# Kernel tuning notes

Hardware: AMD Instinct MI355X
Metric: run time of the kernel (lower is better)

The kernel has to match this reference:

```python
import jax, jax.numpy as jnp
import numpy as np

N = 100_000        # nodes
E = 1_600_000      # edges (avg degree 16)
NODE_DIM = 64
HIDDEN = 64
OUT = 32


def _glorot(key, fan_in, fan_out):
    lim = np.sqrt(6.0 / (fan_in + fan_out)).astype(np.float32)
    return jax.random.uniform(key, (fan_in, fan_out), jnp.float32, -lim, lim)


def setup_inputs() -> dict:
    key = jax.random.key(0)
    ks = jax.random.split(key, 5)
    x = jax.random.normal(ks[0], (N, NODE_DIM), jnp.float32)
    edge_index = jax.random.randint(ks[1], (2, E), 0, N, dtype=jnp.int64)
    return {
        "x": x,
        "edge_index": edge_index,
        "W1": _glorot(ks[2], NODE_DIM, HIDDEN),
        "b1": jnp.zeros((HIDDEN,), jnp.float32),
        "Wmu": _glorot(ks[3], HIDDEN, OUT),
        "bmu": jnp.zeros((OUT,), jnp.float32),
        "Wlv": _glorot(ks[4], HIDDEN, OUT),
        "blv": jnp.zeros((OUT,), jnp.float32),
    }


def _gcn_conv(h, W, b, src, dst, norm, n):
    """PyG GCNConv: linear (no bias) -> normalized scatter-add -> + bias.
    src/dst/norm already include self-loops and deg^{-1/2} symmetric norm."""
    h = h @ W                                   # [n, out]
    msg = h[src] * norm[:, None]                # [E+N, out] gather
    out = jax.ops.segment_sum(msg, dst, num_segments=n)  # scatter-add
    return out + b


def reference(x, edge_index, W1, b1, Wmu, bmu, Wlv, blv):
    loops = jnp.arange(N, dtype=edge_index.dtype)
    src = jnp.concatenate([edge_index[0], loops])  # add self-loops
    dst = jnp.concatenate([edge_index[1], loops])
    # symmetric normalization: deg computed on target nodes (all weights 1)
    deg = jax.ops.segment_sum(jnp.ones_like(src, dtype=x.dtype), dst, num_segments=N)
    dinv = jax.lax.rsqrt(deg)                   # deg >= 1 due to self-loops
    norm = dinv[src] * dinv[dst]

    h = jax.nn.relu(_gcn_conv(x, W1, b1, src, dst, norm, N))
    mu = _gcn_conv(h, Wmu, bmu, src, dst, norm, N)
    logvar = _gcn_conv(h, Wlv, blv, src, dst, norm, N)
    return mu, logvar
```

## Files before the change

### kernel.cpp

```cpp
#include <hip/hip_runtime.h>
#include <hip/hip_fp16.h>


#define BKT_SHIFT 9
#define BKT_NODES 512
#define CHUNK 2048

typedef __attribute__((ext_vector_type(8))) _Float16 half8;
typedef __attribute__((ext_vector_type(4))) float float4v;
typedef __attribute__((ext_vector_type(4))) unsigned uint4v;

__device__ __forceinline__ int imin(int a, int b) { return a < b ? a : b; }
__device__ __forceinline__ int imax(int a, int b) { return a > b ? a : b; }
__device__ __forceinline__ unsigned h2u(__half2 v) {
  union { __half2 h; unsigned u; } c; c.h = v; return c.u;
}
__device__ __forceinline__ __half2 u2h(unsigned x) {
  union { unsigned u; __half2 h; } c; c.u = x; return c.h;
}

__global__ __launch_bounds__(256) void bucket_count(const int* __restrict__ dst,
                                                    int* __restrict__ cnt,
                                                    int E, int nbk, int nblk) {
  __shared__ int hist[2][256];
  const int t = threadIdx.x;
  const int h = (t >> 7) & 1;
  hist[0][t] = 0;
  hist[1][t] = 0;
  __syncthreads();
  const int base = blockIdx.x * CHUNK;
  const int end = imin(base + CHUNK, E);
  for (int e = base + t * 4; e < end; e += 1024) {
    if (e + 3 < end) {
      const int4 d4 = *(const int4*)(dst + e);
      atomicAdd(&hist[h][d4.x >> BKT_SHIFT], 1);
      atomicAdd(&hist[h][d4.y >> BKT_SHIFT], 1);
      atomicAdd(&hist[h][d4.z >> BKT_SHIFT], 1);
      atomicAdd(&hist[h][d4.w >> BKT_SHIFT], 1);
    } else {
      for (int k = e; k < end; ++k) atomicAdd(&hist[h][dst[k] >> BKT_SHIFT], 1);
    }
  }
  __syncthreads();
  if (t < nbk) cnt[t * nblk + blockIdx.x] = hist[0][t] + hist[1][t];
}

__global__ __launch_bounds__(256) void scan_rows(int* __restrict__ cnt,
                                                 int* __restrict__ rowsum,
                                                 int nbk, int nblk) {
  __shared__ int red[256];
  const int b = blockIdx.x;
  const int t = threadIdx.x;
  const int rbase = b * nblk;
  int vals[4];
  int run = 0;
#pragma unroll
  for (int k = 0; k < 4; ++k) {
    const int idx = t * 4 + k;
    const int v = (idx < nblk) ? cnt[rbase + idx] : 0;
    vals[k] = v;
    run += v;
  }
  red[t] = run;
  __syncthreads();
  for (int off = 1; off < 256; off <<= 1) {
    const int u = (t >= off) ? red[t - off] : 0;
    __syncthreads();
    red[t] += u;
    __syncthreads();
  }
  int acc = red[t] - run;
  if (t == 255) rowsum[b] = red[255];
#pragma unroll
  for (int k = 0; k < 4; ++k) {
    const int idx = t * 4 + k;
    if (idx < nblk) {
      cnt[rbase + idx] = acc;
      acc += vals[k];
    }
  }
}

__global__ __launch_bounds__(256) void bucket_scatter(const int* __restrict__ src,
                                                      const int* __restrict__ dst,
                                                      const int* __restrict__ cnt,
                                                      const int* __restrict__ rowsum,
                                                      int* __restrict__ tmp,
                                                      int E, int nbk, int nblk) {
  __shared__ int cur[256];
  __shared__ int red[256];
  const int t = threadIdx.x;
  const int c = blockIdx.x;
  const int v = (t < nbk) ? rowsum[t] : 0;
  red[t] = v;
  __syncthreads();
  for (int off = 1; off < 256; off <<= 1) {
    const int u = (t >= off) ? red[t - off] : 0;
    __syncthreads();
    red[t] += u;
    __syncthreads();
  }
  if (t < nbk) cur[t] = (red[t] - v) + cnt[t * nblk + c];
  __syncthreads();
  const int base = c * CHUNK;
  const int end = imin(base + CHUNK, E);
  for (int e = base + t * 4; e < end; e += 1024) {
    if (e + 3 < end) {
      const int4 s4 = *(const int4*)(src + e);
      const int4 d4 = *(const int4*)(dst + e);
      int p0 = atomicAdd(&cur[d4.x >> BKT_SHIFT], 1);
      tmp[p0] = (s4.x << 9) | (d4.x & 511);
      int p1 = atomicAdd(&cur[d4.y >> BKT_SHIFT], 1);
      tmp[p1] = (s4.y << 9) | (d4.y & 511);
      int p2 = atomicAdd(&cur[d4.z >> BKT_SHIFT], 1);
      tmp[p2] = (s4.z << 9) | (d4.z & 511);
      int p3 = atomicAdd(&cur[d4.w >> BKT_SHIFT], 1);
      tmp[p3] = (s4.w << 9) | (d4.w & 511);
    } else {
      for (int k = e; k < end; ++k) {
        const int d = dst[k];
        const int pos = atomicAdd(&cur[d >> BKT_SHIFT], 1);
        tmp[pos] = (src[k] << 9) | (d & 511);
      }
    }
  }
}

__global__ __launch_bounds__(1024) void bucket_build(const int* __restrict__ tmp,
                                                     const int* __restrict__ rowsum,
                                                     int* __restrict__ row_ptr,
                                                     int* __restrict__ pairs,
                                                     const float* __restrict__ x,
                                                     __half* __restrict__ xs,
                                                     __half* __restrict__ hs,
                                                     int n, int nbk, int E) {
  __shared__ int hist[BKT_NODES];
  __shared__ int scn[BKT_NODES];
  __shared__ int red[256];
  __shared__ int s_sh, e_sh;
  const int b = blockIdx.x;
  const int t = threadIdx.x;
  const int node0 = b << BKT_SHIFT;
  int v0 = 0;
  if (t < 256) {
    v0 = (t < nbk) ? rowsum[t] : 0;
    red[t] = v0;
  }
  if (t < BKT_NODES) hist[t] = 0;
  __syncthreads();
  for (int off = 1; off < 256; off <<= 1) {
    int u = 0;
    if (t < 256 && t >= off) u = red[t - off];
    __syncthreads();
    if (t < 256) red[t] += u;
    __syncthreads();
  }
  if (t == 0) {
    const int incl = red[b];
    e_sh = incl;
    s_sh = incl - rowsum[b];
  }
  __syncthreads();
  const int s = s_sh;
  const int e = e_sh;
  for (int k = s + t; k < e; k += 1024) atomicAdd(&hist[tmp[k] & 511], 1);
  __syncthreads();
  int v = 0;
  if (t < BKT_NODES) {
    v = hist[t];
    scn[t] = v;
  }
  __syncthreads();
  for (int off = 1; off < BKT_NODES; off <<= 1) {
    int u = 0;
    if (t < BKT_NODES && t >= off) u = scn[t - off];
    __syncthreads();
    if (t < BKT_NODES) scn[t] += u;
    __syncthreads();
  }
  if (t < BKT_NODES) {
    const int excl = s + scn[t] - v;
    const int node = node0 + t;
    if (node < n) row_ptr[node] = excl;
    if (b == nbk - 1 && t == 0) row_ptr[n] = E;
    hist[t] = excl;
    scn[t] = __float_as_int(rsqrtf(1.0f + (float)v));
  }
  __syncthreads();
  for (int k = s + t; k < e; k += 1024) {
    const int w = tmp[k];
    const int pos = atomicAdd(&hist[w & 511], 1);
    pairs[pos] = w >> 9;
  }
  const int nloc = imin(BKT_NODES, n - node0);
  for (int idx = t; idx < nloc * 16; idx += 1024) {
    const int nl = idx >> 4, f4 = idx & 15;
    const float4 v4 = ((const float4*)x)[(size_t)(node0 + nl) * 16 + f4];
    const float d = __int_as_float(scn[nl]);
    __half2* o = (__half2*)(xs + (size_t)(node0 + nl) * 64 + f4 * 4);
    o[0] = __floats2half2_rn(d * v4.x, d * v4.y);
    o[1] = __floats2half2_rn(d * v4.z, d * v4.w);
  }
  if (b == 0 && t < 32) {
    if (t < 16)
      ((float2*)(xs + (size_t)n * 64))[t] = make_float2(0.f, 0.f);
    else
      ((float2*)(hs + (size_t)n * 64))[t - 16] = make_float2(0.f, 0.f);
  }
}


#define YSTRIDE 264

__global__ __launch_bounds__(256, 4) void agg_layer1(const __half* __restrict__ xs,
                                                     const int* __restrict__ pairs,
                                                     const int* __restrict__ row_ptr,
                                                     const float* __restrict__ W1,
                                                     const float* __restrict__ b1,
                                                     __half* __restrict__ hs, int n) {
  __shared__ _Float16 ylds_all[4][16 * YSTRIDE];
  __shared__ float dilds_all[4][16];
  const int wv = threadIdx.x >> 6;
  _Float16* ylds = ylds_all[wv];
  float* dilds = dilds_all[wv];
  const int lane = threadIdx.x & 63;
  const int g = lane >> 3, q = lane & 7;
  const int quad = lane >> 4, col = lane & 15;

  half8 bfrag[2][4];
#pragma unroll
  for (int s = 0; s < 2; ++s)
#pragma unroll
    for (int t = 0; t < 4; ++t)
#pragma unroll
      for (int jj = 0; jj < 8; ++jj)
        bfrag[s][t][jj] = (_Float16)W1[(s * 32 + quad * 8 + jj) * 64 + t * 16 + col];
  float bias[4];
#pragma unroll
  for (int t = 0; t < 4; ++t) bias[t] = b1[t * 16 + col];

  const int ntiles = (n + 15) >> 4;
  for (int tile = blockIdx.x * 4 + wv; tile < ntiles; tile += gridDim.x * 4) {
    const int row0 = tile << 4;
#pragma unroll 1
    for (int rg = 0; rg < 4; ++rg) {
      int start[4], end[4], idx[4];
      __half2 acc[4][4];
      int maxdeg = 0;
#pragma unroll
      for (int j = 0; j < 4; ++j) {
        const int i = row0 + rg * 4 + j;
        start[j] = 0; end[j] = 0;
        if (i < n) { start[j] = row_ptr[i]; end[j] = row_ptr[i + 1]; }
        maxdeg = imax(maxdeg, end[j] - start[j]);
#pragma unroll
        for (int k = 0; k < 4; ++k) acc[j][k] = u2h(0u);
        idx[j] = (start[j] + g < end[j]) ? pairs[start[j] + g] : n;
      }
      const int iters = (maxdeg + 7) >> 3;
#pragma unroll 1
      for (int it = 0; it < iters; ++it) {
        int nidx[4];
#pragma unroll
        for (int j = 0; j < 4; ++j) {
          const int ofs2 = start[j] + (it + 1) * 8 + g;
          nidx[j] = (ofs2 < end[j]) ? pairs[ofs2] : n;
        }
#pragma unroll
        for (int j = 0; j < 4; ++j) {
          const float4 rr = *(const float4*)(xs + (size_t)idx[j] * 64 + q * 8);
          const __half2* hp = (const __half2*)&rr;
#pragma unroll
          for (int k = 0; k < 4; ++k) acc[j][k] = __hadd2(acc[j][k], hp[k]);
        }
#pragma unroll
        for (int j = 0; j < 4; ++j) idx[j] = nidx[j];
      }
#pragma unroll
      for (int j = 0; j < 4; ++j) {
        const int i = row0 + rg * 4 + j;
        if (g == 0 && i < n) {
          const float4 sr = *(const float4*)(xs + (size_t)i * 64 + q * 8);
          const __half2* hp = (const __half2*)&sr;
#pragma unroll
          for (int k = 0; k < 4; ++k) acc[j][k] = __hadd2(acc[j][k], hp[k]);
        }
#pragma unroll
        for (int k = 0; k < 4; ++k) {
          unsigned u = __shfl_xor(h2u(acc[j][k]), 32);
          acc[j][k] = __hadd2(acc[j][k], u2h(u));
        }
        const float di = rsqrtf((float)(1 + end[j] - start[j]));
        const __half hdi = __float2half(di);
        const __half2 di2 = __halves2half2(hdi, hdi);
        uint4v st;
        st.x = h2u(__hmul2(di2, acc[j][0]));
        st.y = h2u(__hmul2(di2, acc[j][1]));
        st.z = h2u(__hmul2(di2, acc[j][2]));
        st.w = h2u(__hmul2(di2, acc[j][3]));
        *(uint4v*)(ylds + (rg * 4 + j) * YSTRIDE + (g & 3) * 64 + q * 8) = st;
        if (lane == 0) dilds[rg * 4 + j] = di;
      }
    }
    float4v acc[4];
#pragma unroll
    for (int t = 0; t < 4; ++t) acc[t] = (float4v){bias[t], bias[t], bias[t], bias[t]};
#pragma unroll
    for (int s2 = 0; s2 < 8; ++s2) {
      half8 af = *(half8*)(ylds + col * YSTRIDE + s2 * 32 + quad * 8);
      const int sW = s2 & 1;
#pragma unroll
      for (int t = 0; t < 4; ++t)
        acc[t] = __builtin_amdgcn_mfma_f32_16x16x32_f16(af, bfrag[sW][t], acc[t], 0, 0, 0);
    }
    const float4 dis = *(const float4*)(dilds + quad * 4);
    const float dd[4] = {dis.x, dis.y, dis.z, dis.w};
#pragma unroll
    for (int t = 0; t < 4; ++t)
#pragma unroll
      for (int reg = 0; reg < 4; ++reg) {
        const int row = row0 + quad * 4 + reg;
        if (row < n)
          hs[(size_t)row * 64 + t * 16 + col] =
              __float2half(dd[reg] * fmaxf(acc[t][reg], 0.f));
      }
  }
}

__global__ __launch_bounds__(256, 4) void agg_layer2(const __half* __restrict__ hsin,
                                                     const int* __restrict__ pairs,
                                                     const int* __restrict__ row_ptr,
                                                     const float* __restrict__ Wmu,
                                                     const float* __restrict__ bmu,
                                                     const float* __restrict__ Wlv,
                                                     const float* __restrict__ blv,
                                                     float* __restrict__ out_mu,
                                                     float* __restrict__ out_lv, int n) {
  __shared__ _Float16 ylds_all[4][16 * YSTRIDE];
  const int wv = threadIdx.x >> 6;
  _Float16* ylds = ylds_all[wv];
  const int lane = threadIdx.x & 63;
  const int g = lane >> 3, q = lane & 7;
  const int quad = lane >> 4, col = lane & 15;

  half8 bfrag[2][4];
#pragma unroll
  for (int s = 0; s < 2; ++s)
#pragma unroll
    for (int t = 0; t < 4; ++t) {
      const int j = t * 16 + col;
      const float* W = (j < 32) ? Wmu : Wlv;
      const int jc = j & 31;
#pragma unroll
      for (int jj = 0; jj < 8; ++jj)
        bfrag[s][t][jj] = (_Float16)W[(s * 32 + quad * 8 + jj) * 32 + jc];
    }
  float bias[4];
#pragma unroll
  for (int t = 0; t < 4; ++t) {
    const int j = t * 16 + col;
    bias[t] = (j < 32) ? bmu[j] : blv[j - 32];
  }

  const int ntiles = (n + 15) >> 4;
  for (int tile = blockIdx.x * 4 + wv; tile < ntiles; tile += gridDim.x * 4) {
    const int row0 = tile << 4;
#pragma unroll 1
    for (int rg = 0; rg < 4; ++rg) {
      int start[4], end[4], idx[4];
      __half2 acc[4][4];
      int maxdeg = 0;
#pragma unroll
      for (int j = 0; j < 4; ++j) {
        const int i = row0 + rg * 4 + j;
        start[j] = 0; end[j] = 0;
        if (i < n) { start[j] = row_ptr[i]; end[j] = row_ptr[i + 1]; }
        maxdeg = imax(maxdeg, end[j] - start[j]);
#pragma unroll
        for (int k = 0; k < 4; ++k) acc[j][k] = u2h(0u);
        idx[j] = (start[j] + g < end[j]) ? pairs[start[j] + g] : n;
      }
      const int iters = (maxdeg + 7) >> 3;
#pragma unroll 1
      for (int it = 0; it < iters; ++it) {
        int nidx[4];
#pragma unroll
        for (int j = 0; j < 4; ++j) {
          const int ofs2 = start[j] + (it + 1) * 8 + g;
          nidx[j] = (ofs2 < end[j]) ? pairs[ofs2] : n;
        }
#pragma unroll
        for (int j = 0; j < 4; ++j) {
          const float4 rr = *(const float4*)(hsin + (size_t)idx[j] * 64 + q * 8);
          const __half2* hp = (const __half2*)&rr;
#pragma unroll
          for (int k = 0; k < 4; ++k) acc[j][k] = __hadd2(acc[j][k], hp[k]);
        }
#pragma unroll
        for (int j = 0; j < 4; ++j) idx[j] = nidx[j];
      }
#pragma unroll
      for (int j = 0; j < 4; ++j) {
        const int i = row0 + rg * 4 + j;
        if (g == 0 && i < n) {
          const float4 sr = *(const float4*)(hsin + (size_t)i * 64 + q * 8);
          const __half2* hp = (const __half2*)&sr;
#pragma unroll
          for (int k = 0; k < 4; ++k) acc[j][k] = __hadd2(acc[j][k], hp[k]);
        }
#pragma unroll
        for (int k = 0; k < 4; ++k) {
          unsigned u = __shfl_xor(h2u(acc[j][k]), 32);
          acc[j][k] = __hadd2(acc[j][k], u2h(u));
        }
        const float di = rsqrtf((float)(1 + end[j] - start[j]));
        const __half hdi = __float2half(di);
        const __half2 di2 = __halves2half2(hdi, hdi);
        uint4v st;
        st.x = h2u(__hmul2(di2, acc[j][0]));
        st.y = h2u(__hmul2(di2, acc[j][1]));
        st.z = h2u(__hmul2(di2, acc[j][2]));
        st.w = h2u(__hmul2(di2, acc[j][3]));
        *(uint4v*)(ylds + (rg * 4 + j) * YSTRIDE + (g & 3) * 64 + q * 8) = st;
      }
    }
    float4v acc[4];
#pragma unroll
    for (int t = 0; t < 4; ++t) acc[t] = (float4v){bias[t], bias[t], bias[t], bias[t]};
#pragma unroll
    for (int s2 = 0; s2 < 8; ++s2) {
      half8 af = *(half8*)(ylds + col * YSTRIDE + s2 * 32 + quad * 8);
      const int sW = s2 & 1;
#pragma unroll
      for (int t = 0; t < 4; ++t)
        acc[t] = __builtin_amdgcn_mfma_f32_16x16x32_f16(af, bfrag[sW][t], acc[t], 0, 0, 0);
    }
#pragma unroll
    for (int t = 0; t < 4; ++t)
#pragma unroll
      for (int reg = 0; reg < 4; ++reg) {
        const int row = row0 + quad * 4 + reg;
        if (row < n) {
          const int j = t * 16 + col;
          if (j < 32)
            out_mu[(size_t)row * 32 + j] = acc[t][reg];
          else
            out_lv[(size_t)row * 32 + (j - 32)] = acc[t][reg];
        }
      }
  }
}

extern "C" void kernel_launch(void* const* d_in, const int* in_sizes, int n_in,
                              void* d_out, int out_size, void* d_ws, size_t ws_size,
                              hipStream_t stream) {
  const float* x = (const float*)d_in[0];
  const int* ei = (const int*)d_in[1];
  const float* W1 = (const float*)d_in[2];
  const float* b1 = (const float*)d_in[3];
  const float* Wmu = (const float*)d_in[4];
  const float* bmu = (const float*)d_in[5];
  const float* Wlv = (const float*)d_in[6];
  const float* blv = (const float*)d_in[7];

  const int N = in_sizes[0] / 64;
  const int E = in_sizes[1] / 2;
  const int* src = ei;
  const int* dst = ei + E;

  const int NBK = (N + BKT_NODES - 1) >> BKT_SHIFT;
  const int NBLK = (E + CHUNK - 1) / CHUNK;
  const int FL = NBK * NBLK;

  auto align256 = [](size_t v) { return (v + 255) & ~(size_t)255; };
  char* p = (char*)d_ws;
  int* row_ptr = (int*)p;  p += align256((size_t)(N + 1) * 4);
  int* rowsum = (int*)p;   p += align256((size_t)256 * 4);
  int* cnt = (int*)p;      p += align256((size_t)FL * 4);
  int* pairs = (int*)p;    p += align256((size_t)E * 4);
  __half* xs = (__half*)p; p += align256((size_t)(N + 1) * 64 * 2);
  size_t tmp_bytes = (size_t)E * 4;
  size_t hs_bytes = (size_t)(N + 1) * 64 * 2;
  int* tmp = (int*)p;
  __half* hs = (__half*)p;
  p += align256(tmp_bytes > hs_bytes ? tmp_bytes : hs_bytes);

  float* out_mu = (float*)d_out;
  float* out_lv = out_mu + (size_t)N * 32;

  bucket_count<<<NBLK, 256, 0, stream>>>(dst, cnt, E, NBK, NBLK);
  scan_rows<<<NBK, 256, 0, stream>>>(cnt, rowsum, NBK, NBLK);
  bucket_scatter<<<NBLK, 256, 0, stream>>>(src, dst, cnt, rowsum, tmp, E, NBK, NBLK);
  bucket_build<<<NBK, 1024, 0, stream>>>(tmp, rowsum, row_ptr, pairs, x, xs, hs,
                                         N, NBK, E);

  const int ntiles = (N + 15) / 16;
  const int ablocks = (ntiles + 3) / 4;
  agg_layer1<<<ablocks, 256, 0, stream>>>(xs, pairs, row_ptr, W1, b1, hs, N);
  agg_layer2<<<ablocks, 256, 0, stream>>>(hs, pairs, row_ptr, Wmu, bmu, Wlv, blv,
                                          out_mu, out_lv, N);
}
```

Baseline: 236.6 us.

## Stage bucket scatter and CSR build through shared memory for coalesced writes

bucket_scatter now uses 8192-edge chunks and 512 threads. Each block computes a local histogram, sorts its edges by bucket into LDS, then writes each bucket's run contiguously to global memory instead of issuing random per-edge stores. bucket_build likewise places source indices into an LDS stage, when the bucket fits in STAGE_CAP, and then writes pairs contiguously. This trades extra LDS use, more syncs and a duplicated histogram pass for fewer scattered global writes, with fewer blocks (NBLK presumably shrinks with CHUNK).

```diff
diff --git a/kernel.cpp b/kernel.cpp
--- a/kernel.cpp
+++ b/kernel.cpp
@@ -4,7 +4,8 @@
 
 #define BKT_SHIFT 9
 #define BKT_NODES 512
-#define CHUNK 2048
+#define CHUNK 8192
+#define STAGE_CAP 10240
 
 typedef __attribute__((ext_vector_type(8))) _Float16 half8;
 typedef __attribute__((ext_vector_type(4))) float float4v;
@@ -51,17 +52,8 @@
   __shared__ int red[256];
   const int b = blockIdx.x;
   const int t = threadIdx.x;
-  const int rbase = b * nblk;
-  int vals[4];
-  int run = 0;
-#pragma unroll
-  for (int k = 0; k < 4; ++k) {
-    const int idx = t * 4 + k;
-    const int v = (idx < nblk) ? cnt[rbase + idx] : 0;
-    vals[k] = v;
-    run += v;
-  }
-  red[t] = run;
+  const int v = (t < nblk) ? cnt[b * nblk + t] : 0;
+  red[t] = v;
   __syncthreads();
   for (int off = 1; off < 256; off <<= 1) {
     const int u = (t >= off) ? red[t - off] : 0;
@@ -69,60 +61,101 @@
     red[t] += u;
     __syncthreads();
   }
-  int acc = red[t] - run;
+  if (t < nblk) cnt[b * nblk + t] = red[t] - v;
   if (t == 255) rowsum[b] = red[255];
-#pragma unroll
-  for (int k = 0; k < 4; ++k) {
-    const int idx = t * 4 + k;
-    if (idx < nblk) {
-      cnt[rbase + idx] = acc;
-      acc += vals[k];
-    }
-  }
-}
-
-__global__ __launch_bounds__(256) void bucket_scatter(const int* __restrict__ src,
+}
+
+__global__ __launch_bounds__(512) void bucket_scatter(const int* __restrict__ src,
                                                       const int* __restrict__ dst,
                                                       const int* __restrict__ cnt,
                                                       const int* __restrict__ rowsum,
                                                       int* __restrict__ tmp,
                                                       int E, int nbk, int nblk) {
+  __shared__ int hist[2][256];
+  __shared__ int lofs[256];
+  __shared__ int gofs[256];
   __shared__ int cur[256];
   __shared__ int red[256];
+  __shared__ int stage[CHUNK];
   const int t = threadIdx.x;
   const int c = blockIdx.x;
-  const int v = (t < nbk) ? rowsum[t] : 0;
-  red[t] = v;
-  __syncthreads();
-  for (int off = 1; off < 256; off <<= 1) {
-    const int u = (t >= off) ? red[t - off] : 0;
-    __syncthreads();
-    red[t] += u;
-    __syncthreads();
-  }
-  if (t < nbk) cur[t] = (red[t] - v) + cnt[t * nblk + c];
-  __syncthreads();
+  hist[t >> 8][t & 255] = 0;
+  __syncthreads();
+  const int h = (t >> 8) & 1;
   const int base = c * CHUNK;
   const int end = imin(base + CHUNK, E);
-  for (int e = base + t * 4; e < end; e += 1024) {
+  for (int e = base + t * 4; e < end; e += 2048) {
+    if (e + 3 < end) {
+      const int4 d4 = *(const int4*)(dst + e);
+      atomicAdd(&hist[h][d4.x >> BKT_SHIFT], 1);
+      atomicAdd(&hist[h][d4.y >> BKT_SHIFT], 1);
+      atomicAdd(&hist[h][d4.z >> BKT_SHIFT], 1);
+      atomicAdd(&hist[h][d4.w >> BKT_SHIFT], 1);
+    } else {
+      for (int k = e; k < end; ++k) atomicAdd(&hist[h][dst[k] >> BKT_SHIFT], 1);
+    }
+  }
+  __syncthreads();
+  int tot = 0;
+  if (t < 256) {
+    tot = hist[0][t] + hist[1][t];
+    red[t] = tot;
+  }
+  __syncthreads();
+  for (int off = 1; off < 256; off <<= 1) {
+    int u = 0;
+    if (t < 256 && t >= off) u = red[t - off];
+    __syncthreads();
+    if (t < 256) red[t] += u;
+    __syncthreads();
+  }
+  if (t < 256) {
+    lofs[t] = red[t] - tot;
+    cur[t] = red[t] - tot;
+  }
+  __syncthreads();
+  int rv = 0;
+  if (t < 256) {
+    rv = (t < nbk) ? rowsum[t] : 0;
+    red[t] = rv;
+  }
+  __syncthreads();
+  for (int off = 1; off < 256; off <<= 1) {
+    int u = 0;
+    if (t < 256 && t >= off) u = red[t - off];
+    __syncthreads();
+    if (t < 256) red[t] += u;
+    __syncthreads();
+  }
+  if (t < nbk) gofs[t] = (red[t] - rv) + cnt[t * nblk + c];
+  __syncthreads();
+  for (int e = base + t * 4; e < end; e += 2048) {
     if (e + 3 < end) {
       const int4 s4 = *(const int4*)(src + e);
       const int4 d4 = *(const int4*)(dst + e);
       int p0 = atomicAdd(&cur[d4.x >> BKT_SHIFT], 1);
-      tmp[p0] = (s4.x << 9) | (d4.x & 511);
+      stage[p0] = (s4.x << 9) | (d4.x & 511);
       int p1 = atomicAdd(&cur[d4.y >> BKT_SHIFT], 1);
-      tmp[p1] = (s4.y << 9) | (d4.y & 511);
+      stage[p1] = (s4.y << 9) | (d4.y & 511);
       int p2 = atomicAdd(&cur[d4.z >> BKT_SHIFT], 1);
-      tmp[p2] = (s4.z << 9) | (d4.z & 511);
+      stage[p2] = (s4.z << 9) | (d4.z & 511);
       int p3 = atomicAdd(&cur[d4.w >> BKT_SHIFT], 1);
-      tmp[p3] = (s4.w << 9) | (d4.w & 511);
+      stage[p3] = (s4.w << 9) | (d4.w & 511);
     } else {
       for (int k = e; k < end; ++k) {
         const int d = dst[k];
         const int pos = atomicAdd(&cur[d >> BKT_SHIFT], 1);
-        tmp[pos] = (src[k] << 9) | (d & 511);
-      }
-    }
+        stage[pos] = (src[k] << 9) | (d & 511);
+      }
+    }
+  }
+  __syncthreads();
+  const int wv = t >> 6, lane = t & 63;
+  for (int b = wv; b < nbk; b += 8) {
+    const int len = hist[0][b] + hist[1][b];
+    const int lo = lofs[b];
+    const int go = gofs[b];
+    for (int k = lane; k < len; k += 64) tmp[go + k] = stage[lo + k];
   }
 }
 
@@ -137,7 +170,8 @@
   __shared__ int hist[BKT_NODES];
   __shared__ int scn[BKT_NODES];
   __shared__ int red[256];
-  __shared__ int s_sh, e_sh;
+  __shared__ int stage[STAGE_CAP];
+  __shared__ int s_sh;
   const int b = blockIdx.x;
   const int t = threadIdx.x;
   const int node0 = b << BKT_SHIFT;
@@ -155,14 +189,11 @@
     if (t < 256) red[t] += u;
     __syncthreads();
   }
-  if (t == 0) {
-    const int incl = red[b];
-    e_sh = incl;
-    s_sh = incl - rowsum[b];
-  }
+  if (t == 0) s_sh = red[b] - rowsum[b];
   __syncthreads();
   const int s = s_sh;
-  const int e = e_sh;
+  const int e = s + rowsum[b];
+  const int len = e - s;
   for (int k = s + t; k < e; k += 1024) atomicAdd(&hist[tmp[k] & 511], 1);
   __syncthreads();
   int v = 0;
@@ -178,19 +209,30 @@
     if (t < BKT_NODES) scn[t] += u;
     __syncthreads();
   }
+  const bool staged = (len <= STAGE_CAP);
   if (t < BKT_NODES) {
-    const int excl = s + scn[t] - v;
+    const int lexcl = scn[t] - v;
     const int node = node0 + t;
-    if (node < n) row_ptr[node] = excl;
+    if (node < n) row_ptr[node] = s + lexcl;
     if (b == nbk - 1 && t == 0) row_ptr[n] = E;
-    hist[t] = excl;
+    hist[t] = staged ? lexcl : (s + lexcl);
     scn[t] = __float_as_int(rsqrtf(1.0f + (float)v));
   }
   __syncthreads();
-  for (int k = s + t; k < e; k += 1024) {
-    const int w = tmp[k];
-    const int pos = atomicAdd(&hist[w & 511], 1);
-    pairs[pos] = w >> 9;
+  if (staged) {
+    for (int k = s + t; k < e; k += 1024) {
+      const int w = tmp[k];
+      const int pos = atomicAdd(&hist[w & 511], 1);
+      stage[pos] = w >> 9;
+    }
+    __syncthreads();
+    for (int k = t; k < len; k += 1024) pairs[s + k] = stage[k];
+  } else {
+    for (int k = s + t; k < e; k += 1024) {
+      const int w = tmp[k];
+      const int pos = atomicAdd(&hist[w & 511], 1);
+      pairs[pos] = w >> 9;
+    }
   }
   const int nloc = imin(BKT_NODES, n - node0);
   for (int idx = t; idx < nloc * 16; idx += 1024) {
@@ -490,7 +532,7 @@
 
   bucket_count<<<NBLK, 256, 0, stream>>>(dst, cnt, E, NBK, NBLK);
   scan_rows<<<NBK, 256, 0, stream>>>(cnt, rowsum, NBK, NBLK);
-  bucket_scatter<<<NBLK, 256, 0, stream>>>(src, dst, cnt, rowsum, tmp, E, NBK, NBLK);
+  bucket_scatter<<<NBLK, 512, 0, stream>>>(src, dst, cnt, rowsum, tmp, E, NBK, NBLK);
   bucket_build<<<NBK, 1024, 0, stream>>>(tmp, rowsum, row_ptr, pairs, x, xs, hs,
                                          N, NBK, E);
 
```

After: 229.6 us. 1.03x faster.
